# Kernel tuning notes

Measured on AMD Instinct MI355X. Metric: run time of the kernel, lower is better.

## Reference

```python
import jax, jax.numpy as jnp
import numpy as np

N = 50000
IN_DIM = 512
NEG_SLOPE = 0.2


def gat_conv(x, src, dst, W, a_src, a_dst, bias, heads, out_c, concat):
    # x: [N, F_in]; src/dst: [E] (self-loops already appended)
    n = x.shape[0]
    h = (x @ W).reshape(n, heads, out_c)              # [N,H,C]
    alpha_s = (h * a_src).sum(-1)                     # [N,H]
    alpha_d = (h * a_dst).sum(-1)                     # [N,H]
    e = jax.nn.leaky_relu(alpha_s[src] + alpha_d[dst], NEG_SLOPE)  # [E,H]
    # segment softmax over destination node neighborhoods
    m = jax.ops.segment_max(e, dst, num_segments=n)
    e = jnp.exp(e - m[dst])
    denom = jax.ops.segment_sum(e, dst, num_segments=n)
    alpha = e / (denom[dst] + 1e-16)                  # [E,H]
    msg = h[src] * alpha[:, :, None]                  # [E,H,C]
    out = jax.ops.segment_sum(msg, dst, num_segments=n)  # [N,H,C]
    out = out.reshape(n, heads * out_c) if concat else out.mean(axis=1)
    return out + bias


def setup_inputs() -> dict:
    key = jax.random.key(0)
    ks = jax.random.split(key, 16)
    E = 1600000
    txt = jax.random.normal(ks[0], (N, 768), dtype=jnp.float32)
    x = jax.random.normal(ks[1], (N, IN_DIM), dtype=jnp.float32)
    edge_index = jax.random.randint(ks[2], (2, E), 0, N, dtype=jnp.int64)
    s = lambda fan: 1.0 / np.sqrt(fan)
    W1 = jax.random.normal(ks[3], (IN_DIM, 4 * 32), dtype=jnp.float32) * s(IN_DIM)
    a_src1 = jax.random.normal(ks[4], (4, 32), dtype=jnp.float32) * s(32)
    a_dst1 = jax.random.normal(ks[5], (4, 32), dtype=jnp.float32) * s(32)
    b1 = jnp.zeros((4 * 32,), dtype=jnp.float32)
    W2 = jax.random.normal(ks[6], (128, 32), dtype=jnp.float32) * s(128)
    a_src2 = jax.random.normal(ks[7], (1, 32), dtype=jnp.float32) * s(32)
    a_dst2 = jax.random.normal(ks[8], (1, 32), dtype=jnp.float32) * s(32)
    b2 = jnp.zeros((32,), dtype=jnp.float32)
    Wf1 = jax.random.normal(ks[9], (768 + 32, 64), dtype=jnp.float32) * s(800)
    bf1 = jnp.zeros((64,), dtype=jnp.float32)
    Wf2 = jax.random.normal(ks[10], (64, 1), dtype=jnp.float32) * s(64)
    bf2 = jnp.zeros((1,), dtype=jnp.float32)
    return {"txt": txt, "x": x, "W1": W1, "a_src1": a_src1, "a_dst1": a_dst1,
            "b1": b1, "W2": W2, "a_src2": a_src2, "a_dst2": a_dst2, "b2": b2,
            "Wf1": Wf1, "bf1": bf1, "Wf2": Wf2, "bf2": bf2,
            "edge_index": edge_index}


def reference(txt, x, W1, a_src1, a_dst1, b1, W2, a_src2, a_dst2, b2,
              Wf1, bf1, Wf2, bf2, edge_index):
    # PyG GATConv adds self-loops by default
    loops = jnp.arange(N, dtype=edge_index.dtype)
    src = jnp.concatenate([edge_index[0], loops])
    dst = jnp.concatenate([edge_index[1], loops])
    h1 = gat_conv(x, src, dst, W1, a_src1, a_dst1, b1, 4, 32, True)    # [N,128]
    h1 = jax.nn.elu(h1)
    g = gat_conv(h1, src, dst, W2, a_src2, a_dst2, b2, 1, 32, False)   # [N,32]
    z = jnp.concatenate([txt, g], axis=1)                              # [N,800]
    z = jax.nn.relu(z @ Wf1 + bf1)
    out = (z @ Wf2 + bf2).squeeze(-1)                                  # [N]
    return out
```

## Files before the change

### kernel.cpp

```cpp
#include <hip/hip_runtime.h>
#include <hip/hip_bf16.h>
#include <cstdint>

#define NEG_SLOPE 0.2f
#define BCAP 16384

typedef __bf16 bf16_t;
typedef __bf16 bf16x8 __attribute__((ext_vector_type(8)));
typedef float f32x4 __attribute__((ext_vector_type(4)));
typedef float f32x2 __attribute__((ext_vector_type(2)));

__device__ __forceinline__ uint2 pack4bf16(float4 v) {
    ushort u0 = __builtin_bit_cast(ushort, (bf16_t)v.x);
    ushort u1 = __builtin_bit_cast(ushort, (bf16_t)v.y);
    ushort u2 = __builtin_bit_cast(ushort, (bf16_t)v.z);
    ushort u3 = __builtin_bit_cast(ushort, (bf16_t)v.w);
    uint2 r;
    r.x = (uint)u0 | ((uint)u1 << 16);
    r.y = (uint)u2 | ((uint)u3 << 16);
    return r;
}

__device__ __forceinline__ float bflo(uint u) { return __builtin_bit_cast(float, u << 16); }
__device__ __forceinline__ float bfhi(uint u) { return __builtin_bit_cast(float, u & 0xFFFF0000u); }

__global__ __launch_bounds__(256) void k_bucket(const int* __restrict__ ei, int E, int n,
                                                int nbuck, unsigned* __restrict__ gcur,
                                                unsigned* __restrict__ gbuck) {
    __shared__ unsigned stage[4096];
    __shared__ unsigned cnt[256], sc[256], offx[256], gbase[256];
    int tid = threadIdx.x;
    int ET = E + n;
    int tileStart = blockIdx.x * 4096;
    cnt[tid] = 0;
    __syncthreads();
    unsigned pk[16];
    int rk[16];
    #pragma unroll
    for (int i = 0; i < 16; ++i) {
        int idx = tileStart + i * 256 + tid;
        rk[i] = -1;
        if (idx < ET) {
            int s, d;
            if (idx < E) { s = ei[idx]; d = ei[E + idx]; } else { s = d = idx - E; }
            pk[i] = ((unsigned)d << 16) | (unsigned)s;
            rk[i] = (int)atomicAdd(&cnt[(unsigned)d >> 8], 1u);
        }
    }
    __syncthreads();
    sc[tid] = cnt[tid];
    __syncthreads();
    for (int off = 1; off < 256; off <<= 1) {
        unsigned t = (tid >= off) ? sc[tid - off] : 0u;
        __syncthreads();
        sc[tid] += t;
        __syncthreads();
    }
    offx[tid] = sc[tid] - cnt[tid];
    if (tid < nbuck && cnt[tid] > 0) gbase[tid] = atomicAdd(&gcur[tid], cnt[tid]);
    unsigned total = sc[255];
    __syncthreads();
    #pragma unroll
    for (int i = 0; i < 16; ++i) {
        if (rk[i] >= 0) stage[offx[pk[i] >> 24] + rk[i]] = pk[i];
    }
    __syncthreads();
    for (unsigned j = tid; j < total; j += 256) {
        unsigned p = stage[j];
        unsigned b = p >> 24;
        unsigned pos = gbase[b] + (j - offx[b]);
        gbuck[(size_t)b * BCAP + pos] = p;
    }
}

__global__ __launch_bounds__(256) void k_finecsr(const unsigned* __restrict__ gcur,
                                                 const unsigned* __restrict__ gbuck,
                                                 int nbuck,
                                                 unsigned* __restrict__ rowptr,
                                                 ushort* __restrict__ csr16) {
    __shared__ unsigned s[256];
    __shared__ unsigned c[256], sc[256], cur[256];
    int b = blockIdx.x;
    int tid = threadIdx.x;
    unsigned v = (tid < nbuck) ? gcur[tid] : 0u;
    s[tid] = v;
    __syncthreads();
    for (int off = 1; off < 256; off <<= 1) {
        unsigned t = (tid >= off) ? s[tid - off] : 0u;
        __syncthreads();
        s[tid] += t;
        __syncthreads();
    }
    unsigned base = s[b] - gcur[b];
    unsigned cntL = gcur[b];
    const unsigned* gb = gbuck + (size_t)b * BCAP;
    c[tid] = 0;
    __syncthreads();
    for (unsigned j = tid; j < cntL; j += 256) atomicAdd(&c[(gb[j] >> 16) & 255], 1u);
    __syncthreads();
    sc[tid] = c[tid];
    __syncthreads();
    for (int off = 1; off < 256; off <<= 1) {
        unsigned t = (tid >= off) ? sc[tid - off] : 0u;
        __syncthreads();
        sc[tid] += t;
        __syncthreads();
    }
    unsigned ox = sc[tid] - c[tid];
    rowptr[b * 256 + tid] = base + ox;
    cur[tid] = ox;
    __syncthreads();
    for (unsigned j = tid; j < cntL; j += 256) {
        unsigned p = gb[j];
        unsigned dl = (p >> 16) & 255;
        unsigned pos = atomicAdd(&cur[dl], 1u);
        csr16[base + pos] = (ushort)(p & 0xFFFFu);
    }
}

__global__ __launch_bounds__(256) void k_w1t(const float* __restrict__ W, bf16_t* __restrict__ Wt) {
    __shared__ float s[16][17];
    int tx = threadIdx.x & 15, ty = threadIdx.x >> 4;
    int kt = blockIdx.x & 31, nt = blockIdx.x >> 5;
    s[ty][tx] = W[(size_t)(kt * 16 + ty) * 128 + nt * 16 + tx];
    __syncthreads();
    Wt[(size_t)(nt * 16 + ty) * 512 + kt * 16 + tx] = (bf16_t)s[tx][ty];
}

__global__ __launch_bounds__(256) void k_wf1t(const float* __restrict__ W, bf16_t* __restrict__ Wt) {
    __shared__ float s[16][17];
    int tx = threadIdx.x & 15, ty = threadIdx.x >> 4;
    int kt = blockIdx.x % 52, nt = blockIdx.x / 52;
    int kg = kt * 16 + ty;
    s[ty][tx] = (kg < 800) ? W[(size_t)kg * 64 + nt * 16 + tx] : 0.f;
    __syncthreads();
    Wt[(size_t)(nt * 16 + ty) * 832 + kt * 16 + tx] = (bf16_t)s[tx][ty];
}

__global__ __launch_bounds__(256) void k_gemm1_mfma(const float* __restrict__ x,
                                                    const bf16_t* __restrict__ W1bt,
                                                    const float* __restrict__ a_src1,
                                                    const float* __restrict__ a_dst1,
                                                    unsigned char* __restrict__ h1f8,
                                                    float* __restrict__ asrc,
                                                    float* __restrict__ adst, int n) {
    __shared__ char lds[24576];
    char* As = lds;
    char* Bs = lds + 8192;
    int tid = threadIdx.x;
    int bn = blockIdx.x * 64;
    int wave = tid >> 6, lane = tid & 63;
    int lr = lane & 15, lk = lane >> 4;
    f32x4 acc[8] = {};
    const float4* x4 = (const float4*)x;

    for (int s = 0; s < 8; ++s) {
        int k0 = s * 64;
        #pragma unroll
        for (int i = 0; i < 4; ++i) {
            int v = tid + i * 256;
            int row = v >> 4, c4 = v & 15;
            int node = bn + row;
            float4 val = (node < n) ? x4[(size_t)node * 128 + (k0 >> 2) + c4]
                                    : make_float4(0.f, 0.f, 0.f, 0.f);
            uint off = (uint)(row * 128 + c4 * 8);
            off ^= (uint)((row & 7) << 4);
            *(uint2*)(As + off) = pack4bf16(val);
        }
        #pragma unroll
        for (int i = 0; i < 8; ++i) {
            int v = tid + i * 256;
            int row = v >> 4, c = v & 15;
            uint2 val = *(const uint2*)(W1bt + (size_t)row * 512 + k0 + c * 4);
            uint off = (uint)(row * 128 + c * 8);
            off ^= (uint)((row & 7) << 4);
            *(uint2*)(Bs + off) = val;
        }
        __syncthreads();
        #pragma unroll
        for (int ks = 0; ks < 2; ++ks) {
            uint arow = (uint)(wave * 16 + lr);
            uint aoff = (arow * 128 + (uint)(ks * 64 + lk * 16)) ^ (uint)((lr & 7) << 4);
            bf16x8 av = *(const bf16x8*)(As + aoff);
            #pragma unroll
            for (int f = 0; f < 8; ++f) {
                uint brow = (uint)(f * 16 + lr);
                uint boff = (brow * 128 + (uint)(ks * 64 + lk * 16)) ^ (uint)((lr & 7) << 4);
                bf16x8 bv = *(const bf16x8*)(Bs + boff);
                acc[f] = __builtin_amdgcn_mfma_f32_16x16x32_bf16(av, bv, acc[f], 0, 0, 0);
            }
        }
        __syncthreads();
    }
    #pragma unroll
    for (int f = 0; f < 8; ++f) {
        int nn = f * 16 + lr;
        #pragma unroll
        for (int r = 0; r < 4; ++r) {
            int node = bn + wave * 16 + lk * 4 + r;
            if (node < n) {
                float v = acc[f][r];
                uint b8 = (uint)__builtin_amdgcn_cvt_pk_fp8_f32(v, v, 0, false) & 0xFFu;
                h1f8[(size_t)node * 128 + nn] = (unsigned char)b8;
            }
        }
    }
    float asv[8], adv[8];
    #pragma unroll
    for (int h = 0; h < 4; ++h) {
        asv[2 * h]     = a_src1[h * 32 + lr];
        asv[2 * h + 1] = a_src1[h * 32 + 16 + lr];
        adv[2 * h]     = a_dst1[h * 32 + lr];
        adv[2 * h + 1] = a_dst1[h * 32 + 16 + lr];
    }
    #pragma unroll
    for (int r = 0; r < 4; ++r) {
        int node = bn + wave * 16 + lk * 4 + r;
        #pragma unroll
        for (int h = 0; h < 4; ++h) {
            float ps = acc[2 * h][r] * asv[2 * h] + acc[2 * h + 1][r] * asv[2 * h + 1];
            float pd = acc[2 * h][r] * adv[2 * h] + acc[2 * h + 1][r] * adv[2 * h + 1];
            #pragma unroll
            for (int m = 8; m >= 1; m >>= 1) {
                ps += __shfl_xor(ps, m, 64);
                pd += __shfl_xor(pd, m, 64);
            }
            if (node < n) {
                if (lr == h)     asrc[node * 4 + h] = ps;
                if (lr == h + 4) adst[node * 4 + h] = pd;
            }
        }
    }
}

__global__ __launch_bounds__(512, 8) void k_gat1(const unsigned char* __restrict__ h1f8,
                                                 const float* __restrict__ asrc,
                                                 const float* __restrict__ adst,
                                                 const float* __restrict__ b1,
                                                 const unsigned* __restrict__ rowptr,
                                                 const ushort* __restrict__ csr16,
                                                 const float* __restrict__ W2,
                                                 const float* __restrict__ a_src2,
                                                 const float* __restrict__ a_dst2,
                                                 bf16_t* __restrict__ h2bf,
                                                 float* __restrict__ asrc2,
                                                 float* __restrict__ adst2, int n) {
    __shared__ float W2l[128 * 32];
    __shared__ ushort ssm[8][64];
    __shared__ float psm[8][64][4];
    int tid = threadIdx.x;
    {
        const float4* w4 = (const float4*)W2;
        float4* wl4 = (float4*)W2l;
        #pragma unroll
        for (int i = 0; i < 2; ++i) wl4[tid + i * 512] = w4[tid + i * 512];
    }
    __syncthreads();
    int wv = tid >> 6, l = tid & 63;
    int d = blockIdx.x * 8 + wv;
    if (d >= n) return;
    ushort* ss = ssm[wv];
    unsigned k0 = rowptr[d], k1 = rowptr[d + 1];
    float4 ad4 = *(const float4*)(adst + (size_t)d * 4);
    const float4* asrc4 = (const float4*)asrc;
    const uint2* h1u2 = (const uint2*)h1f8;
    int c16 = l & 15, sub = l >> 4;
    int hd = c16 >> 2;
    float den0 = 0.f, den1 = 0.f, den2 = 0.f, den3 = 0.f;
    float a[8] = {};
    for (unsigned kk = k0; kk < k1; kk += 64) {
        unsigned k = kk + l;
        float p0 = 0.f, p1 = 0.f, p2 = 0.f, p3 = 0.f;
        unsigned s = 0u;
        if (k < k1) {
            s = csr16[k];
            float4 av = asrc4[s];
            float v0 = av.x + ad4.x; v0 = (v0 > 0.f) ? v0 : NEG_SLOPE * v0; p0 = __expf(v0);
            float v1 = av.y + ad4.y; v1 = (v1 > 0.f) ? v1 : NEG_SLOPE * v1; p1 = __expf(v1);
            float v2 = av.z + ad4.z; v2 = (v2 > 0.f) ? v2 : NEG_SLOPE * v2; p2 = __expf(v2);
            float v3 = av.w + ad4.w; v3 = (v3 > 0.f) ? v3 : NEG_SLOPE * v3; p3 = __expf(v3);
        }
        ss[l] = (ushort)s;
        float4 pv; pv.x = p0; pv.y = p1; pv.z = p2; pv.w = p3;
        *(float4*)psm[wv][l] = pv;
        den0 += p0; den1 += p1; den2 += p2; den3 += p3;
        int nk = (int)min(64u, k1 - kk);
        for (int qb = 0; qb < nk; qb += 4) {
            int q = qb + sub;
            float pq = psm[wv][q][hd];
            unsigned sq = ss[q];
            uint2 u = h1u2[sq * 16u + (unsigned)c16];
            f32x2 v0 = __builtin_amdgcn_cvt_pk_f32_fp8(u.x, false);
            f32x2 v1 = __builtin_amdgcn_cvt_pk_f32_fp8(u.x, true);
            f32x2 v2 = __builtin_amdgcn_cvt_pk_f32_fp8(u.y, false);
            f32x2 v3 = __builtin_amdgcn_cvt_pk_f32_fp8(u.y, true);
            a[0] = fmaf(pq, v0.x, a[0]); a[1] = fmaf(pq, v0.y, a[1]);
            a[2] = fmaf(pq, v1.x, a[2]); a[3] = fmaf(pq, v1.y, a[3]);
            a[4] = fmaf(pq, v2.x, a[4]); a[5] = fmaf(pq, v2.y, a[5]);
            a[6] = fmaf(pq, v3.x, a[6]); a[7] = fmaf(pq, v3.y, a[7]);
        }
    }
    #pragma unroll
    for (int m = 32; m >= 1; m >>= 1) {
        den0 += __shfl_xor(den0, m, 64);
        den1 += __shfl_xor(den1, m, 64);
        den2 += __shfl_xor(den2, m, 64);
        den3 += __shfl_xor(den3, m, 64);
    }
    #pragma unroll
    for (int i = 0; i < 8; ++i) {
        a[i] += __shfl_xor(a[i], 16, 64);
        a[i] += __shfl_xor(a[i], 32, 64);
    }
    float denh = (hd == 0) ? den0 : (hd == 1) ? den1 : (hd == 2) ? den2 : den3;
    float inv = 1.f / (denh + 1e-16f);
    float* os = (float*)psm[wv];
    if (sub == 0) {
        float4 ba = *(const float4*)(b1 + 8 * c16);
        float4 bbv = *(const float4*)(b1 + 8 * c16 + 4);
        float o0 = a[0] * inv + ba.x;  o0 = (o0 > 0.f) ? o0 : (__expf(o0) - 1.f);
        float o1 = a[1] * inv + ba.y;  o1 = (o1 > 0.f) ? o1 : (__expf(o1) - 1.f);
        float o2 = a[2] * inv + ba.z;  o2 = (o2 > 0.f) ? o2 : (__expf(o2) - 1.f);
        float o3 = a[3] * inv + ba.w;  o3 = (o3 > 0.f) ? o3 : (__expf(o3) - 1.f);
        float o4 = a[4] * inv + bbv.x; o4 = (o4 > 0.f) ? o4 : (__expf(o4) - 1.f);
        float o5 = a[5] * inv + bbv.y; o5 = (o5 > 0.f) ? o5 : (__expf(o5) - 1.f);
        float o6 = a[6] * inv + bbv.z; o6 = (o6 > 0.f) ? o6 : (__expf(o6) - 1.f);
        float o7 = a[7] * inv + bbv.w; o7 = (o7 > 0.f) ? o7 : (__expf(o7) - 1.f);
        float4 ov0; ov0.x = o0; ov0.y = o1; ov0.z = o2; ov0.w = o3;
        float4 ov1; ov1.x = o4; ov1.y = o5; ov1.z = o6; ov1.w = o7;
        *(float4*)(os + 8 * c16) = ov0;
        *(float4*)(os + 8 * c16 + 4) = ov1;
    }
    int j32 = l & 31, kh = l >> 5;
    float part = 0.f;
    const float4* os4 = (const float4*)(os + kh * 64);
    #pragma unroll 4
    for (int i = 0; i < 16; ++i) {
        float4 ov = os4[i];
        int kb = kh * 64 + i * 4;
        part += ov.x * W2l[(kb + 0) * 32 + j32] + ov.y * W2l[(kb + 1) * 32 + j32]
              + ov.z * W2l[(kb + 2) * 32 + j32] + ov.w * W2l[(kb + 3) * 32 + j32];
    }
    part += __shfl_xor(part, 32, 64);
    float h2v = part;
    float cs = h2v * a_src2[j32];
    float cd = h2v * a_dst2[j32];
    #pragma unroll
    for (int m = 16; m >= 1; m >>= 1) {
        cs += __shfl_xor(cs, m, 64);
        cd += __shfl_xor(cd, m, 64);
    }
    if (l < 32) h2bf[(size_t)d * 32 + l] = (bf16_t)h2v;
    if (l == 0) { asrc2[d] = cs; adst2[d] = cd; }
}

__global__ __launch_bounds__(256, 8) void k_gat2(const bf16_t* __restrict__ h2bf,
                                                 const float* __restrict__ asrc2,
                                                 const float* __restrict__ adst2,
                                                 const float* __restrict__ b2,
                                                 const unsigned* __restrict__ rowptr,
                                                 const ushort* __restrict__ csr16,
                                                 float* __restrict__ g, int n) {
    __shared__ ushort ssm[4][64];
    __shared__ float psm[4][64];
    int tid = threadIdx.x;
    int wv = tid >> 6, l = tid & 63;
    int d = blockIdx.x * 4 + wv;
    if (d >= n) return;
    ushort* ss = ssm[wv];
    float* ps = psm[wv];
    unsigned k0 = rowptr[d], k1 = rowptr[d + 1];
    float adh = adst2[d];
    const uint2* h2u2 = (const uint2*)h2bf;
    int c = l & 7, sub = l >> 3;
    float den = 0.f, a0 = 0.f, a1 = 0.f, a2 = 0.f, a3 = 0.f;
    for (unsigned kk = k0; kk < k1; kk += 64) {
        unsigned k = kk + l;
        float p = 0.f;
        unsigned s = 0u;
        if (k < k1) {
            s = csr16[k];
            float v = asrc2[s] + adh;
            v = (v > 0.f) ? v : NEG_SLOPE * v;
            p = __expf(v);
        }
        ss[l] = (ushort)s;
        ps[l] = p;
        den += p;
        int nk = (int)min(64u, k1 - kk);
        for (int qb = 0; qb < nk; qb += 8) {
            int q = qb + sub;
            float pq = ps[q];
            uint2 u = h2u2[(unsigned)ss[q] * 8u + (unsigned)c];
            a0 = fmaf(pq, bflo(u.x), a0);
            a1 = fmaf(pq, bfhi(u.x), a1);
            a2 = fmaf(pq, bflo(u.y), a2);
            a3 = fmaf(pq, bfhi(u.y), a3);
        }
    }
    #pragma unroll
    for (int m = 32; m >= 1; m >>= 1) den += __shfl_xor(den, m, 64);
    #pragma unroll
    for (int m = 8; m <= 32; m <<= 1) {
        a0 += __shfl_xor(a0, m, 64);
        a1 += __shfl_xor(a1, m, 64);
        a2 += __shfl_xor(a2, m, 64);
        a3 += __shfl_xor(a3, m, 64);
    }
    if (l < 8) {
        float inv = 1.f / (den + 1e-16f);
        float4 bb = *(const float4*)(b2 + 4 * c);
        float4 val;
        val.x = a0 * inv + bb.x;
        val.y = a1 * inv + bb.y;
        val.z = a2 * inv + bb.z;
        val.w = a3 * inv + bb.w;
        *(float4*)(g + (size_t)d * 32 + 4 * c) = val;
    }
}

__global__ __launch_bounds__(256) void k_mlp_mfma(const float* __restrict__ txt,
                                                  const float* __restrict__ g,
                                                  const bf16_t* __restrict__ Wf1bt,
                                                  const float* __restrict__ bf1,
                                                  const float* __restrict__ Wf2,
                                                  const float* __restrict__ bf2,
                                                  float* __restrict__ out, int n) {
    __shared__ char lds[16384];
    char* As = lds;
    char* Bs = lds + 8192;
    int tid = threadIdx.x;
    int bn = blockIdx.x * 64;
    int wave = tid >> 6, lane = tid & 63;
    int lr = lane & 15, lk = lane >> 4;
    f32x4 acc[4] = {};
    const float4* t4 = (const float4*)txt;
    const float4* g4 = (const float4*)g;

    for (int s = 0; s < 13; ++s) {
        int k0 = s * 64;
        #pragma unroll
        for (int i = 0; i < 4; ++i) {
            int v = tid + i * 256;
            int row = v >> 4, c4 = v & 15;
            int node = bn + row;
            int kg = k0 + c4 * 4;
            float4 val = make_float4(0.f, 0.f, 0.f, 0.f);
            if (node < n) {
                if (kg < 768)      val = t4[(size_t)node * 192 + (kg >> 2)];
                else if (kg < 800) val = g4[(size_t)node * 8 + ((kg - 768) >> 2)];
            }
            uint off = (uint)(row * 128 + c4 * 8);
            off ^= (uint)((row & 7) << 4);
            *(uint2*)(As + off) = pack4bf16(val);
        }
        #pragma unroll
        for (int i = 0; i < 4; ++i) {
            int v = tid + i * 256;
            int row = v >> 4, c = v & 15;
            uint2 val = *(const uint2*)(Wf1bt + (size_t)row * 832 + k0 + c * 4);
            uint off = (uint)(row * 128 + c * 8);
            off ^= (uint)((row & 7) << 4);
            *(uint2*)(Bs + off) = val;
        }
        __syncthreads();
        #pragma unroll
        for (int ks = 0; ks < 2; ++ks) {
            uint arow = (uint)(wave * 16 + lr);
            uint aoff = (arow * 128 + (uint)(ks * 64 + lk * 16)) ^ (uint)((lr & 7) << 4);
            bf16x8 av = *(const bf16x8*)(As + aoff);
            #pragma unroll
            for (int f = 0; f < 4; ++f) {
                uint brow = (uint)(f * 16 + lr);
                uint boff = (brow * 128 + (uint)(ks * 64 + lk * 16)) ^ (uint)((lr & 7) << 4);
                bf16x8 bv = *(const bf16x8*)(Bs + boff);
                acc[f] = __builtin_amdgcn_mfma_f32_16x16x32_bf16(av, bv, acc[f], 0, 0, 0);
            }
        }
        __syncthreads();
    }
    float rsum[4] = {0.f, 0.f, 0.f, 0.f};
    #pragma unroll
    for (int f = 0; f < 4; ++f) {
        int nn = f * 16 + lr;
        float bb = bf1[nn], ww = Wf2[nn];
        #pragma unroll
        for (int r = 0; r < 4; ++r) {
            float v = acc[f][r] + bb;
            rsum[r] += fmaxf(v, 0.f) * ww;
        }
    }
    #pragma unroll
    for (int r = 0; r < 4; ++r) {
        #pragma unroll
        for (int m = 8; m >= 1; m >>= 1) rsum[r] += __shfl_xor(rsum[r], m, 64);
        if (lr == 0) {
            int node = bn + wave * 16 + lk * 4 + r;
            if (node < n) out[node] = rsum[r] + bf2[0];
        }
    }
}

extern "C" void kernel_launch(void* const* d_in, const int* in_sizes, int n_in,
                              void* d_out, int out_size, void* d_ws, size_t ws_size,
                              hipStream_t stream) {
    const float* txt    = (const float*)d_in[0];
    const float* x      = (const float*)d_in[1];
    const float* W1     = (const float*)d_in[2];
    const float* a_src1 = (const float*)d_in[3];
    const float* a_dst1 = (const float*)d_in[4];
    const float* b1     = (const float*)d_in[5];
    const float* W2     = (const float*)d_in[6];
    const float* a_src2 = (const float*)d_in[7];
    const float* a_dst2 = (const float*)d_in[8];
    const float* b2     = (const float*)d_in[9];
    const float* Wf1    = (const float*)d_in[10];
    const float* bf1    = (const float*)d_in[11];
    const float* Wf2    = (const float*)d_in[12];
    const float* bf2    = (const float*)d_in[13];
    const int*   ei     = (const int*)d_in[14];

    int n  = in_sizes[1] / 512;
    int E  = in_sizes[14] / 2;
    int ET = E + n;
    int nbuck = (n + 255) >> 8;
    float* out = (float*)d_out;

    char* p = (char*)d_ws;
    auto alloc = [&](size_t bytes) -> char* {
        char* q = p;
        p += (bytes + 255) & ~(size_t)255;
        return q;
    };
    unsigned char* h1f8 = (unsigned char*)alloc((size_t)n * 128);
    float*    asrc1  = (float*)alloc((size_t)n * 4 * 4);
    float*    adst1  = (float*)alloc((size_t)n * 4 * 4);
    bf16_t*   h2bf   = (bf16_t*)alloc((size_t)n * 32 * 2);
    float*    asrc2  = (float*)alloc((size_t)n * 4);
    float*    adst2  = (float*)alloc((size_t)n * 4);
    float*    gbuf   = (float*)alloc((size_t)n * 32 * 4);
    unsigned* rowptr = (unsigned*)alloc((size_t)(nbuck * 256 + 1) * 4);
    ushort*   csr16  = (ushort*)alloc((size_t)ET * 2);
    unsigned* gbuck  = (unsigned*)alloc((size_t)nbuck * BCAP * 4);
    unsigned* gcur   = (unsigned*)alloc((size_t)nbuck * 4);
    bf16_t*   W1bt   = (bf16_t*)alloc((size_t)128 * 512 * 2);
    bf16_t*   Wf1bt  = (bf16_t*)alloc((size_t)64 * 832 * 2);

    hipMemsetAsync(gcur, 0, (size_t)nbuck * 4, stream);

    k_w1t<<<256, 256, 0, stream>>>(W1, W1bt);
    k_wf1t<<<208, 256, 0, stream>>>(Wf1, Wf1bt);

    int ntiles = (ET + 4095) / 4096;
    k_bucket<<<ntiles, 256, 0, stream>>>(ei, E, n, nbuck, gcur, gbuck);
    k_finecsr<<<nbuck, 256, 0, stream>>>(gcur, gbuck, nbuck, rowptr, csr16);

    int nb64 = (n + 63) / 64;
    int nb8 = (n + 7) / 8;
    int nb4 = (n + 3) / 4;
    k_gemm1_mfma<<<nb64, 256, 0, stream>>>(x, W1bt, a_src1, a_dst1, h1f8, asrc1, adst1, n);
    k_gat1<<<nb8, 512, 0, stream>>>(h1f8, asrc1, adst1, b1, rowptr, csr16,
                                    W2, a_src2, a_dst2, h2bf, asrc2, adst2, n);
    k_gat2<<<nb4, 256, 0, stream>>>(h2bf, asrc2, adst2, b2, rowptr, csr16, gbuf, n);
    k_mlp_mfma<<<nb64, 256, 0, stream>>>(txt, gbuf, Wf1bt, bf1, Wf2, bf2, out, n);
}
```

Measured before the change: 244.5 us.

## Merge independent kernels into combined launches and split MLP into txt and g parts

Independent stages are packed into single launches that pick their role from the block index: bucketing plus both weight transposes, fine CSR build plus the first GEMM, and the txt part of the MLP plus the second GAT layer. The MLP is split so the 768-wide txt GEMM runs alongside GAT2, and a small follow-up kernel adds the 32-wide g contribution and the epilogue. This cuts launch count and serialization between stages. The cost is an extra n×64 fp32 partial-sum buffer written and read back, and larger LDS per block in the merged kernels.

```diff
diff --git a/kernel.cpp b/kernel.cpp
--- a/kernel.cpp
+++ b/kernel.cpp
@@ -24,14 +24,17 @@
 __device__ __forceinline__ float bflo(uint u) { return __builtin_bit_cast(float, u << 16); }
 __device__ __forceinline__ float bfhi(uint u) { return __builtin_bit_cast(float, u & 0xFFFF0000u); }
 
-__global__ __launch_bounds__(256) void k_bucket(const int* __restrict__ ei, int E, int n,
-                                                int nbuck, unsigned* __restrict__ gcur,
-                                                unsigned* __restrict__ gbuck) {
-    __shared__ unsigned stage[4096];
-    __shared__ unsigned cnt[256], sc[256], offx[256], gbase[256];
+
+__device__ void bucket_dev(char* smem, int b, const int* __restrict__ ei, int E, int n,
+                           int nbuck, unsigned* __restrict__ gcur, unsigned* __restrict__ gbuck) {
+    unsigned* stage = (unsigned*)smem;
+    unsigned* cnt   = stage + 4096;
+    unsigned* sc    = cnt + 256;
+    unsigned* offx  = sc + 256;
+    unsigned* gbase = offx + 256;
     int tid = threadIdx.x;
     int ET = E + n;
-    int tileStart = blockIdx.x * 4096;
+    int tileStart = b * 4096;
     cnt[tid] = 0;
     __syncthreads();
     unsigned pk[16];
@@ -67,20 +70,38 @@
     __syncthreads();
     for (unsigned j = tid; j < total; j += 256) {
         unsigned p = stage[j];
-        unsigned b = p >> 24;
-        unsigned pos = gbase[b] + (j - offx[b]);
-        gbuck[(size_t)b * BCAP + pos] = p;
-    }
-}
-
-__global__ __launch_bounds__(256) void k_finecsr(const unsigned* __restrict__ gcur,
-                                                 const unsigned* __restrict__ gbuck,
-                                                 int nbuck,
-                                                 unsigned* __restrict__ rowptr,
-                                                 ushort* __restrict__ csr16) {
-    __shared__ unsigned s[256];
-    __shared__ unsigned c[256], sc[256], cur[256];
-    int b = blockIdx.x;
+        unsigned bb = p >> 24;
+        unsigned pos = gbase[bb] + (j - offx[bb]);
+        gbuck[(size_t)bb * BCAP + pos] = p;
+    }
+}
+
+__device__ void w1t_dev(char* smem, int b, const float* __restrict__ W, bf16_t* __restrict__ Wt) {
+    float (*s)[17] = (float(*)[17])smem;
+    int tx = threadIdx.x & 15, ty = threadIdx.x >> 4;
+    int kt = b & 31, nt = b >> 5;
+    s[ty][tx] = W[(size_t)(kt * 16 + ty) * 128 + nt * 16 + tx];
+    __syncthreads();
+    Wt[(size_t)(nt * 16 + ty) * 512 + kt * 16 + tx] = (bf16_t)s[tx][ty];
+}
+
+__device__ void wf1t_dev(char* smem, int b, const float* __restrict__ W, bf16_t* __restrict__ Wt) {
+    float (*s)[17] = (float(*)[17])smem;
+    int tx = threadIdx.x & 15, ty = threadIdx.x >> 4;
+    int kt = b % 52, nt = b / 52;
+    int kg = kt * 16 + ty;
+    s[ty][tx] = (kg < 800) ? W[(size_t)kg * 64 + nt * 16 + tx] : 0.f;
+    __syncthreads();
+    Wt[(size_t)(nt * 16 + ty) * 832 + kt * 16 + tx] = (bf16_t)s[tx][ty];
+}
+
+__device__ void finecsr_dev(char* smem, int b, const unsigned* __restrict__ gcur,
+                            const unsigned* __restrict__ gbuck, int nbuck,
+                            unsigned* __restrict__ rowptr, ushort* __restrict__ csr16) {
+    unsigned* s   = (unsigned*)smem;
+    unsigned* c   = s + 256;
+    unsigned* sc  = c + 256;
+    unsigned* cur = sc + 256;
     int tid = threadIdx.x;
     unsigned v = (tid < nbuck) ? gcur[tid] : 0u;
     s[tid] = v;
@@ -118,37 +139,15 @@
     }
 }
 
-__global__ __launch_bounds__(256) void k_w1t(const float* __restrict__ W, bf16_t* __restrict__ Wt) {
-    __shared__ float s[16][17];
-    int tx = threadIdx.x & 15, ty = threadIdx.x >> 4;
-    int kt = blockIdx.x & 31, nt = blockIdx.x >> 5;
-    s[ty][tx] = W[(size_t)(kt * 16 + ty) * 128 + nt * 16 + tx];
-    __syncthreads();
-    Wt[(size_t)(nt * 16 + ty) * 512 + kt * 16 + tx] = (bf16_t)s[tx][ty];
-}
-
-__global__ __launch_bounds__(256) void k_wf1t(const float* __restrict__ W, bf16_t* __restrict__ Wt) {
-    __shared__ float s[16][17];
-    int tx = threadIdx.x & 15, ty = threadIdx.x >> 4;
-    int kt = blockIdx.x % 52, nt = blockIdx.x / 52;
-    int kg = kt * 16 + ty;
-    s[ty][tx] = (kg < 800) ? W[(size_t)kg * 64 + nt * 16 + tx] : 0.f;
-    __syncthreads();
-    Wt[(size_t)(nt * 16 + ty) * 832 + kt * 16 + tx] = (bf16_t)s[tx][ty];
-}
-
-__global__ __launch_bounds__(256) void k_gemm1_mfma(const float* __restrict__ x,
-                                                    const bf16_t* __restrict__ W1bt,
-                                                    const float* __restrict__ a_src1,
-                                                    const float* __restrict__ a_dst1,
-                                                    unsigned char* __restrict__ h1f8,
-                                                    float* __restrict__ asrc,
-                                                    float* __restrict__ adst, int n) {
-    __shared__ char lds[24576];
-    char* As = lds;
-    char* Bs = lds + 8192;
+__device__ void gemm1_dev(char* smem, int b, const float* __restrict__ x,
+                          const bf16_t* __restrict__ W1bt,
+                          const float* __restrict__ a_src1, const float* __restrict__ a_dst1,
+                          unsigned char* __restrict__ h1f8,
+                          float* __restrict__ asrc, float* __restrict__ adst, int n) {
+    char* As = smem;
+    char* Bs = smem + 8192;
     int tid = threadIdx.x;
-    int bn = blockIdx.x * 64;
+    int bn = b * 64;
     int wave = tid >> 6, lane = tid & 63;
     int lr = lane & 15, lk = lane >> 4;
     f32x4 acc[8] = {};
@@ -231,6 +230,178 @@
             }
         }
     }
+}
+
+__device__ void mlpA_dev(char* smem, int b, const float* __restrict__ txt,
+                         const bf16_t* __restrict__ Wf1bt, float* __restrict__ hacc, int n) {
+    char* As = smem;
+    char* Bs = smem + 8192;
+    int tid = threadIdx.x;
+    int bn = b * 64;
+    int wave = tid >> 6, lane = tid & 63;
+    int lr = lane & 15, lk = lane >> 4;
+    f32x4 acc[4] = {};
+    const float4* t4 = (const float4*)txt;
+    for (int s = 0; s < 12; ++s) {
+        int k0 = s * 64;
+        #pragma unroll
+        for (int i = 0; i < 4; ++i) {
+            int v = tid + i * 256;
+            int row = v >> 4, c4 = v & 15;
+            int node = bn + row;
+            int kg = k0 + c4 * 4;
+            float4 val = (node < n) ? t4[(size_t)node * 192 + (kg >> 2)]
+                                    : make_float4(0.f, 0.f, 0.f, 0.f);
+            uint off = (uint)(row * 128 + c4 * 8);
+            off ^= (uint)((row & 7) << 4);
+            *(uint2*)(As + off) = pack4bf16(val);
+        }
+        #pragma unroll
+        for (int i = 0; i < 4; ++i) {
+            int v = tid + i * 256;
+            int row = v >> 4, c = v & 15;
+            uint2 val = *(const uint2*)(Wf1bt + (size_t)row * 832 + k0 + c * 4);
+            uint off = (uint)(row * 128 + c * 8);
+            off ^= (uint)((row & 7) << 4);
+            *(uint2*)(Bs + off) = val;
+        }
+        __syncthreads();
+        #pragma unroll
+        for (int ks = 0; ks < 2; ++ks) {
+            uint arow = (uint)(wave * 16 + lr);
+            uint aoff = (arow * 128 + (uint)(ks * 64 + lk * 16)) ^ (uint)((lr & 7) << 4);
+            bf16x8 av = *(const bf16x8*)(As + aoff);
+            #pragma unroll
+            for (int f = 0; f < 4; ++f) {
+                uint brow = (uint)(f * 16 + lr);
+                uint boff = (brow * 128 + (uint)(ks * 64 + lk * 16)) ^ (uint)((lr & 7) << 4);
+                bf16x8 bv = *(const bf16x8*)(Bs + boff);
+                acc[f] = __builtin_amdgcn_mfma_f32_16x16x32_bf16(av, bv, acc[f], 0, 0, 0);
+            }
+        }
+        __syncthreads();
+    }
+    #pragma unroll
+    for (int f = 0; f < 4; ++f) {
+        int nn = f * 16 + lr;
+        #pragma unroll
+        for (int r = 0; r < 4; ++r) {
+            int node = bn + wave * 16 + lk * 4 + r;
+            if (node < n) hacc[(size_t)node * 64 + nn] = acc[f][r];
+        }
+    }
+}
+
+__device__ void gat2_dev(char* smem, int b, const bf16_t* __restrict__ h2bf,
+                         const float* __restrict__ asrc2, const float* __restrict__ adst2,
+                         const float* __restrict__ b2, const unsigned* __restrict__ rowptr,
+                         const ushort* __restrict__ csr16, float* __restrict__ g, int n) {
+    ushort* ssm = (ushort*)smem;
+    float* psm = (float*)(smem + 512);
+    int tid = threadIdx.x;
+    int wv = tid >> 6, l = tid & 63;
+    int d = b * 4 + wv;
+    if (d >= n) return;
+    ushort* ss = ssm + wv * 64;
+    float* ps = psm + wv * 64;
+    unsigned k0 = rowptr[d], k1 = rowptr[d + 1];
+    float adh = adst2[d];
+    const uint2* h2u2 = (const uint2*)h2bf;
+    int c = l & 7, sub = l >> 3;
+    float den = 0.f, a0 = 0.f, a1 = 0.f, a2 = 0.f, a3 = 0.f;
+    for (unsigned kk = k0; kk < k1; kk += 64) {
+        unsigned k = kk + l;
+        float p = 0.f;
+        unsigned s = 0u;
+        if (k < k1) {
+            s = csr16[k];
+            float v = asrc2[s] + adh;
+            v = (v > 0.f) ? v : NEG_SLOPE * v;
+            p = __expf(v);
+        }
+        ss[l] = (ushort)s;
+        ps[l] = p;
+        den += p;
+        int nk = (int)min(64u, k1 - kk);
+        for (int qb = 0; qb < nk; qb += 8) {
+            int q = qb + sub;
+            float pq = ps[q];
+            uint2 u = h2u2[(unsigned)ss[q] * 8u + (unsigned)c];
+            a0 = fmaf(pq, bflo(u.x), a0);
+            a1 = fmaf(pq, bfhi(u.x), a1);
+            a2 = fmaf(pq, bflo(u.y), a2);
+            a3 = fmaf(pq, bfhi(u.y), a3);
+        }
+    }
+    #pragma unroll
+    for (int m = 32; m >= 1; m >>= 1) den += __shfl_xor(den, m, 64);
+    #pragma unroll
+    for (int m = 8; m <= 32; m <<= 1) {
+        a0 += __shfl_xor(a0, m, 64);
+        a1 += __shfl_xor(a1, m, 64);
+        a2 += __shfl_xor(a2, m, 64);
+        a3 += __shfl_xor(a3, m, 64);
+    }
+    if (l < 8) {
+        float inv = 1.f / (den + 1e-16f);
+        float4 bb = *(const float4*)(b2 + 4 * c);
+        float4 val;
+        val.x = a0 * inv + bb.x;
+        val.y = a1 * inv + bb.y;
+        val.z = a2 * inv + bb.z;
+        val.w = a3 * inv + bb.w;
+        *(float4*)(g + (size_t)d * 32 + 4 * c) = val;
+    }
+}
+
+
+__global__ __launch_bounds__(256) void k_fuse_pre(const int* __restrict__ ei, int E, int n,
+                                                  int nbuck, int ntiles,
+                                                  unsigned* __restrict__ gcur,
+                                                  unsigned* __restrict__ gbuck,
+                                                  const float* __restrict__ W1,
+                                                  bf16_t* __restrict__ W1bt,
+                                                  const float* __restrict__ Wf1,
+                                                  bf16_t* __restrict__ Wf1bt) {
+    __shared__ __align__(16) char smem[20480];
+    int b = blockIdx.x;
+    if (b < ntiles)            bucket_dev(smem, b, ei, E, n, nbuck, gcur, gbuck);
+    else if (b < ntiles + 256) w1t_dev(smem, b - ntiles, W1, W1bt);
+    else                       wf1t_dev(smem, b - ntiles - 256, Wf1, Wf1bt);
+}
+
+__global__ __launch_bounds__(256) void k_fuse_csr_gemm(const unsigned* __restrict__ gcur,
+                                                       const unsigned* __restrict__ gbuck,
+                                                       int nbuck,
+                                                       unsigned* __restrict__ rowptr,
+                                                       ushort* __restrict__ csr16,
+                                                       const float* __restrict__ x,
+                                                       const bf16_t* __restrict__ W1bt,
+                                                       const float* __restrict__ a_src1,
+                                                       const float* __restrict__ a_dst1,
+                                                       unsigned char* __restrict__ h1f8,
+                                                       float* __restrict__ asrc,
+                                                       float* __restrict__ adst, int n) {
+    __shared__ __align__(16) char smem[24576];
+    int b = blockIdx.x;
+    if (b < nbuck) finecsr_dev(smem, b, gcur, gbuck, nbuck, rowptr, csr16);
+    else           gemm1_dev(smem, b - nbuck, x, W1bt, a_src1, a_dst1, h1f8, asrc, adst, n);
+}
+
+__global__ __launch_bounds__(256) void k_fuse_mlpA_gat2(const float* __restrict__ txt,
+                                                        const bf16_t* __restrict__ Wf1bt,
+                                                        float* __restrict__ hacc, int nb64,
+                                                        const bf16_t* __restrict__ h2bf,
+                                                        const float* __restrict__ asrc2,
+                                                        const float* __restrict__ adst2,
+                                                        const float* __restrict__ b2,
+                                                        const unsigned* __restrict__ rowptr,
+                                                        const ushort* __restrict__ csr16,
+                                                        float* __restrict__ g, int n) {
+    __shared__ __align__(16) char smem[16384];
+    int b = blockIdx.x;
+    if (b < nb64) mlpA_dev(smem, b, txt, Wf1bt, hacc, n);
+    else          gat2_dev(smem, b - nb64, h2bf, asrc2, adst2, b2, rowptr, csr16, g, n);
 }
 
 __global__ __launch_bounds__(512, 8) void k_gat1(const unsigned char* __restrict__ h1f8,
@@ -354,130 +525,65 @@
     if (l == 0) { asrc2[d] = cs; adst2[d] = cd; }
 }
 
-__global__ __launch_bounds__(256, 8) void k_gat2(const bf16_t* __restrict__ h2bf,
-                                                 const float* __restrict__ asrc2,
-                                                 const float* __restrict__ adst2,
-                                                 const float* __restrict__ b2,
-                                                 const unsigned* __restrict__ rowptr,
-                                                 const ushort* __restrict__ csr16,
-                                                 float* __restrict__ g, int n) {
-    __shared__ ushort ssm[4][64];
-    __shared__ float psm[4][64];
-    int tid = threadIdx.x;
-    int wv = tid >> 6, l = tid & 63;
-    int d = blockIdx.x * 4 + wv;
-    if (d >= n) return;
-    ushort* ss = ssm[wv];
-    float* ps = psm[wv];
-    unsigned k0 = rowptr[d], k1 = rowptr[d + 1];
-    float adh = adst2[d];
-    const uint2* h2u2 = (const uint2*)h2bf;
-    int c = l & 7, sub = l >> 3;
-    float den = 0.f, a0 = 0.f, a1 = 0.f, a2 = 0.f, a3 = 0.f;
-    for (unsigned kk = k0; kk < k1; kk += 64) {
-        unsigned k = kk + l;
-        float p = 0.f;
-        unsigned s = 0u;
-        if (k < k1) {
-            s = csr16[k];
-            float v = asrc2[s] + adh;
-            v = (v > 0.f) ? v : NEG_SLOPE * v;
-            p = __expf(v);
-        }
-        ss[l] = (ushort)s;
-        ps[l] = p;
-        den += p;
-        int nk = (int)min(64u, k1 - kk);
-        for (int qb = 0; qb < nk; qb += 8) {
-            int q = qb + sub;
-            float pq = ps[q];
-            uint2 u = h2u2[(unsigned)ss[q] * 8u + (unsigned)c];
-            a0 = fmaf(pq, bflo(u.x), a0);
-            a1 = fmaf(pq, bfhi(u.x), a1);
-            a2 = fmaf(pq, bflo(u.y), a2);
-            a3 = fmaf(pq, bfhi(u.y), a3);
-        }
-    }
-    #pragma unroll
-    for (int m = 32; m >= 1; m >>= 1) den += __shfl_xor(den, m, 64);
-    #pragma unroll
-    for (int m = 8; m <= 32; m <<= 1) {
-        a0 += __shfl_xor(a0, m, 64);
-        a1 += __shfl_xor(a1, m, 64);
-        a2 += __shfl_xor(a2, m, 64);
-        a3 += __shfl_xor(a3, m, 64);
-    }
-    if (l < 8) {
-        float inv = 1.f / (den + 1e-16f);
-        float4 bb = *(const float4*)(b2 + 4 * c);
-        float4 val;
-        val.x = a0 * inv + bb.x;
-        val.y = a1 * inv + bb.y;
-        val.z = a2 * inv + bb.z;
-        val.w = a3 * inv + bb.w;
-        *(float4*)(g + (size_t)d * 32 + 4 * c) = val;
-    }
-}
-
-__global__ __launch_bounds__(256) void k_mlp_mfma(const float* __restrict__ txt,
-                                                  const float* __restrict__ g,
-                                                  const bf16_t* __restrict__ Wf1bt,
-                                                  const float* __restrict__ bf1,
-                                                  const float* __restrict__ Wf2,
-                                                  const float* __restrict__ bf2,
-                                                  float* __restrict__ out, int n) {
-    __shared__ char lds[16384];
-    char* As = lds;
-    char* Bs = lds + 8192;
+__global__ __launch_bounds__(256) void k_mlpB(const float* __restrict__ g,
+                                              const bf16_t* __restrict__ Wf1bt,
+                                              const float* __restrict__ hacc,
+                                              const float* __restrict__ bf1,
+                                              const float* __restrict__ Wf2,
+                                              const float* __restrict__ bf2,
+                                              float* __restrict__ out, int n) {
+    __shared__ __align__(16) char smem[16384];
+    char* As = smem;
+    char* Bs = smem + 8192;
     int tid = threadIdx.x;
     int bn = blockIdx.x * 64;
     int wave = tid >> 6, lane = tid & 63;
     int lr = lane & 15, lk = lane >> 4;
-    f32x4 acc[4] = {};
-    const float4* t4 = (const float4*)txt;
     const float4* g4 = (const float4*)g;
-
-    for (int s = 0; s < 13; ++s) {
-        int k0 = s * 64;
-        #pragma unroll
-        for (int i = 0; i < 4; ++i) {
-            int v = tid + i * 256;
-            int row = v >> 4, c4 = v & 15;
-            int node = bn + row;
-            int kg = k0 + c4 * 4;
-            float4 val = make_float4(0.f, 0.f, 0.f, 0.f);
-            if (node < n) {
-                if (kg < 768)      val = t4[(size_t)node * 192 + (kg >> 2)];
-                else if (kg < 800) val = g4[(size_t)node * 8 + ((kg - 768) >> 2)];
-            }
-            uint off = (uint)(row * 128 + c4 * 8);
-            off ^= (uint)((row & 7) << 4);
-            *(uint2*)(As + off) = pack4bf16(val);
-        }
-        #pragma unroll
-        for (int i = 0; i < 4; ++i) {
-            int v = tid + i * 256;
-            int row = v >> 4, c = v & 15;
-            uint2 val = *(const uint2*)(Wf1bt + (size_t)row * 832 + k0 + c * 4);
-            uint off = (uint)(row * 128 + c * 8);
-            off ^= (uint)((row & 7) << 4);
-            *(uint2*)(Bs + off) = val;
-        }
-        __syncthreads();
-        #pragma unroll
-        for (int ks = 0; ks < 2; ++ks) {
-            uint arow = (uint)(wave * 16 + lr);
-            uint aoff = (arow * 128 + (uint)(ks * 64 + lk * 16)) ^ (uint)((lr & 7) << 4);
-            bf16x8 av = *(const bf16x8*)(As + aoff);
-            #pragma unroll
-            for (int f = 0; f < 4; ++f) {
-                uint brow = (uint)(f * 16 + lr);
-                uint boff = (brow * 128 + (uint)(ks * 64 + lk * 16)) ^ (uint)((lr & 7) << 4);
-                bf16x8 bv = *(const bf16x8*)(Bs + boff);
-                acc[f] = __builtin_amdgcn_mfma_f32_16x16x32_bf16(av, bv, acc[f], 0, 0, 0);
-            }
-        }
-        __syncthreads();
+    #pragma unroll
+    for (int i = 0; i < 4; ++i) {
+        int v = tid + i * 256;
+        int row = v >> 4, c4 = v & 15;
+        int node = bn + row;
+        int kg = 768 + c4 * 4;
+        float4 val = make_float4(0.f, 0.f, 0.f, 0.f);
+        if (node < n && kg < 800) val = g4[(size_t)node * 8 + ((kg - 768) >> 2)];
+        uint off = (uint)(row * 128 + c4 * 8);
+        off ^= (uint)((row & 7) << 4);
+        *(uint2*)(As + off) = pack4bf16(val);
+    }
+    #pragma unroll
+    for (int i = 0; i < 4; ++i) {
+        int v = tid + i * 256;
+        int row = v >> 4, c = v & 15;
+        uint2 val = *(const uint2*)(Wf1bt + (size_t)row * 832 + 768 + c * 4);
+        uint off = (uint)(row * 128 + c * 8);
+        off ^= (uint)((row & 7) << 4);
+        *(uint2*)(Bs + off) = val;
+    }
+    f32x4 acc[4];
+    #pragma unroll
+    for (int f = 0; f < 4; ++f) {
+        int nn = f * 16 + lr;
+        #pragma unroll
+        for (int r = 0; r < 4; ++r) {
+            int node = bn + wave * 16 + lk * 4 + r;
+            acc[f][r] = (node < n) ? hacc[(size_t)node * 64 + nn] : 0.f;
+        }
+    }
+    __syncthreads();
+    #pragma unroll
+    for (int ks = 0; ks < 2; ++ks) {
+        uint arow = (uint)(wave * 16 + lr);
+        uint aoff = (arow * 128 + (uint)(ks * 64 + lk * 16)) ^ (uint)((lr & 7) << 4);
+        bf16x8 av = *(const bf16x8*)(As + aoff);
+        #pragma unroll
+        for (int f = 0; f < 4; ++f) {
+            uint brow = (uint)(f * 16 + lr);
+            uint boff = (brow * 128 + (uint)(ks * 64 + lk * 16)) ^ (uint)((lr & 7) << 4);
+            bf16x8 bv = *(const bf16x8*)(Bs + boff);
+            acc[f] = __builtin_amdgcn_mfma_f32_16x16x32_bf16(av, bv, acc[f], 0, 0, 0);
+        }
     }
     float rsum[4] = {0.f, 0.f, 0.f, 0.f};
     #pragma unroll
@@ -539,6 +645,7 @@
     float*    asrc2  = (float*)alloc((size_t)n * 4);
     float*    adst2  = (float*)alloc((size_t)n * 4);
     float*    gbuf   = (float*)alloc((size_t)n * 32 * 4);
+    float*    hacc   = (float*)alloc((size_t)n * 64 * 4);
     unsigned* rowptr = (unsigned*)alloc((size_t)(nbuck * 256 + 1) * 4);
     ushort*   csr16  = (ushort*)alloc((size_t)ET * 2);
     unsigned* gbuck  = (unsigned*)alloc((size_t)nbuck * BCAP * 4);
@@ -548,19 +655,20 @@
 
     hipMemsetAsync(gcur, 0, (size_t)nbuck * 4, stream);
 
-    k_w1t<<<256, 256, 0, stream>>>(W1, W1bt);
-    k_wf1t<<<208, 256, 0, stream>>>(Wf1, Wf1bt);
-
     int ntiles = (ET + 4095) / 4096;
-    k_bucket<<<ntiles, 256, 0, stream>>>(ei, E, n, nbuck, gcur, gbuck);
-    k_finecsr<<<nbuck, 256, 0, stream>>>(gcur, gbuck, nbuck, rowptr, csr16);
-
     int nb64 = (n + 63) / 64;
     int nb8 = (n + 7) / 8;
     int nb4 = (n + 3) / 4;
-    k_gemm1_mfma<<<nb64, 256, 0, stream>>>(x, W1bt, a_src1, a_dst1, h1f8, asrc1, adst1, n);
+
+    k_fuse_pre<<<ntiles + 256 + 208, 256, 0, stream>>>(ei, E, n, nbuck, ntiles,
+                                                       gcur, gbuck, W1, W1bt, Wf1, Wf1bt);
+    k_fuse_csr_gemm<<<nbuck + nb64, 256, 0, stream>>>(gcur, gbuck, nbuck, rowptr, csr16,
+                                                      x, W1bt, a_src1, a_dst1, h1f8,
+                                                      asrc1, adst1, n);
     k_gat1<<<nb8, 512, 0, stream>>>(h1f8, asrc1, adst1, b1, rowptr, csr16,
                                     W2, a_src2, a_dst2, h2bf, asrc2, adst2, n);
-    k_gat2<<<nb4, 256, 0, stream>>>(h2bf, asrc2, adst2, b2, rowptr, csr16, gbuf, n);
-    k_mlp_mfma<<<nb64, 256, 0, stream>>>(txt, gbuf, Wf1bt, bf1, Wf2, bf2, out, n);
-}
+    k_fuse_mlpA_gat2<<<nb64 + nb4, 256, 0, stream>>>(txt, Wf1bt, hacc, nb64,
+                                                     h2bf, asrc2, adst2, b2,
+                                                     rowptr, csr16, gbuf, n);
+    k_mlpB<<<nb64, 256, 0, stream>>>(gbuf, Wf1bt, hacc, bf1, Wf2, bf2, out, n);
+}
```

Result: faster. 205.1 us (-16.1%).
